# Optimization experiments

Hardware: AMD Instinct MI355X
Metric: run time of the kernel (lower is better)

Reference implementation:

```python
import jax, jax.numpy as jnp
import numpy as np

N, E, G = 50000, 800000, 64          # nodes, edges, graphs
IN, HID, OUT, H = 256, 64, 64, 4     # input dim, per-head hidden, output dim, heads
NEG_SLOPE = 0.2                      # PyG GATConv leaky_relu slope


def _lin(k, fan_in, fan_out):
    return jax.random.normal(k, (fan_in, fan_out), jnp.float32) * (1.0 / np.sqrt(fan_in))


def setup_inputs() -> dict:
    key = jax.random.key(0)
    ks = jax.random.split(key, 16)
    x = jax.random.normal(ks[0], (N, IN), jnp.float32)
    edge_index = jax.random.randint(ks[1], (2, E), 0, N, dtype=jnp.int32)
    batch = jnp.sort(jax.random.randint(ks[2], (N,), 0, G, dtype=jnp.int32))
    # layer 1: IN -> H x HID (concat)
    W1 = _lin(ks[3], IN, H * HID)
    a_src1 = jax.random.normal(ks[4], (H, HID), jnp.float32) * 0.1
    a_dst1 = jax.random.normal(ks[5], (H, HID), jnp.float32) * 0.1
    b1 = jnp.zeros((H * HID,), jnp.float32)
    # layer 2: H*HID -> H x HID (concat)
    W2 = _lin(ks[6], H * HID, H * HID)
    a_src2 = jax.random.normal(ks[7], (H, HID), jnp.float32) * 0.1
    a_dst2 = jax.random.normal(ks[8], (H, HID), jnp.float32) * 0.1
    b2 = jnp.zeros((H * HID,), jnp.float32)
    W3 = _lin(ks[9], H * HID, OUT)
    a_src3 = jax.random.normal(ks[10], (1, OUT), jnp.float32) * 0.1
    a_dst3 = jax.random.normal(ks[11], (1, OUT), jnp.float32) * 0.1
    b3 = jnp.zeros((OUT,), jnp.float32)
    return {"x": x, "edge_index": edge_index, "batch": batch,
            "W1": W1, "a_src1": a_src1, "a_dst1": a_dst1, "b1": b1,
            "W2": W2, "a_src2": a_src2, "a_dst2": a_dst2, "b2": b2,
            "W3": W3, "a_src3": a_src3, "a_dst3": a_dst3, "b3": b3}


def gat_conv(x, src, dst, W, a_src, a_dst, b, heads, out_ch):
    """PyG-style GATConv (eval mode, concat=True semantics; heads=1 == no concat)."""
    n = x.shape[0]
    h = (x @ W).reshape(n, heads, out_ch)                     # [N,H,C]
    alpha_s = jnp.sum(h * a_src, axis=-1)                     # [N,H]
    alpha_d = jnp.sum(h * a_dst, axis=-1)                     # [N,H]
    e = jax.nn.leaky_relu(alpha_s[src] + alpha_d[dst], NEG_SLOPE)  # [E',H]
    # segment softmax over destination nodes (self-loops guarantee nonempty segments)
    m = jax.ops.segment_max(e, dst, num_segments=n)
    e = jnp.exp(e - m[dst])
    denom = jax.ops.segment_sum(e, dst, num_segments=n)
    alpha = e / (denom[dst] + 1e-16)                          # [E',H]
    msg = h[src] * alpha[:, :, None]                          # [E',H,C]
    out = jax.ops.segment_sum(msg, dst, num_segments=n)       # [N,H,C]
    return out.reshape(n, heads * out_ch) + b


def reference(x, edge_index, batch, W1, a_src1, a_dst1, b1, W2, a_src2, a_dst2, b2,
              W3, a_src3, a_dst3, b3):
    n = x.shape[0]
    # GATConv default add_self_loops=True
    loops = jnp.arange(n, dtype=edge_index.dtype)
    src = jnp.concatenate([edge_index[0], loops])
    dst = jnp.concatenate([edge_index[1], loops])

    h = gat_conv(x, src, dst, W1, a_src1, a_dst1, b1, H, HID)
    h = jax.nn.elu(h)  # dropout disabled in eval
    h = gat_conv(h, src, dst, W2, a_src2, a_dst2, b2, H, HID)
    h = jax.nn.elu(h)
    node_embeddings = gat_conv(h, src, dst, W3, a_src3, a_dst3, b3, 1, OUT)

    # global_mean_pool over batch ids
    sums = jax.ops.segment_sum(node_embeddings, batch, num_segments=G)
    counts = jax.ops.segment_sum(jnp.ones((n,), node_embeddings.dtype), batch, num_segments=G)
    graph_embeddings = sums / jnp.maximum(counts, 1.0)[:, None]
    return node_embeddings, graph_embeddings
```

## Files before the change

kernel.cpp:

```cpp
#include <hip/hip_runtime.h>
#include <hip/hip_bf16.h>
#include <hip/hip_fp16.h>

typedef __attribute__((ext_vector_type(8))) _Float16 f16x8;
typedef __attribute__((ext_vector_type(4))) _Float16 f16x4;
typedef __attribute__((ext_vector_type(4))) float f32x4;

static __device__ __forceinline__ void st(float* p, float v)  { *p = v; }
static __device__ __forceinline__ void st(__half* p, float v) { *p = __float2half(v); }

static __device__ __forceinline__ void splitf16(float v, __half& hi, __half& lo) {
    hi = __float2half(v);
    lo = __float2half(v - __half2float(hi));
}

static __device__ __forceinline__ void ldrow4(const __half* p, float* f) {
    const __half2* q = reinterpret_cast<const __half2*>(p);
    float2 a = __half22float2(q[0]), b = __half22float2(q[1]);
    f[0] = a.x; f[1] = a.y; f[2] = b.x; f[3] = b.y;
}
template <int CHUNK>
static __device__ __forceinline__ void ldrow(const __half* p, float* f) {
    if constexpr (CHUNK == 4) ldrow4(p, f); else f[0] = __half2float(*p);
}

__global__ void k_init(int* deg, int N) {
    int i = blockIdx.x * blockDim.x + threadIdx.x;
    if (i < N) deg[i] = 1;
}

__global__ void k_hist(const int* __restrict__ ei, int* deg, int E) {
    int e = blockIdx.x * blockDim.x + threadIdx.x;
    if (e < E) atomicAdd(&deg[ei[E + e]], 1);
}

__global__ void k_scan1(const int* __restrict__ deg, int* __restrict__ offs,
                        int* __restrict__ bsum, int N) {
    __shared__ int sh[256];
    int i = blockIdx.x * 256 + threadIdx.x;
    int v = (i < N) ? deg[i] : 0;
    sh[threadIdx.x] = v;
    __syncthreads();
#pragma unroll
    for (int off = 1; off < 256; off <<= 1) {
        int t = (threadIdx.x >= off) ? sh[threadIdx.x - off] : 0;
        __syncthreads();
        sh[threadIdx.x] += t;
        __syncthreads();
    }
    if (i < N) offs[i] = sh[threadIdx.x] - v;
    if (threadIdx.x == 255) bsum[blockIdx.x] = sh[255];
}

__global__ void k_scan2(int* __restrict__ bsum, int nb) {
    __shared__ int sh[256];
    int v = (threadIdx.x < nb) ? bsum[threadIdx.x] : 0;
    sh[threadIdx.x] = v;
    __syncthreads();
#pragma unroll
    for (int off = 1; off < 256; off <<= 1) {
        int t = (threadIdx.x >= off) ? sh[threadIdx.x - off] : 0;
        __syncthreads();
        sh[threadIdx.x] += t;
        __syncthreads();
    }
    if (threadIdx.x < nb) bsum[threadIdx.x] = sh[threadIdx.x] - v;
    if (threadIdx.x == 255) bsum[nb] = sh[255];
}

__global__ void k_scan3(int* __restrict__ offs, int* __restrict__ cursor,
                        const int* __restrict__ bsum, int N, int nb) {
    int i = blockIdx.x * 256 + threadIdx.x;
    if (i < N) {
        int v = offs[i] + bsum[blockIdx.x];
        offs[i] = v;
        cursor[i] = v;
    }
    if (i == 0) offs[N] = bsum[nb];
}

__global__ void k_scatter(const int* __restrict__ ei, int* cursor, int* csr, int E) {
    int e = blockIdx.x * blockDim.x + threadIdx.x;
    if (e < E) {
        int d = ei[E + e];
        int p = atomicAdd(&cursor[d], 1);
        csr[p] = ei[e];
    }
}

__global__ void k_scatter_loops(int* cursor, int* csr, int N) {
    int i = blockIdx.x * blockDim.x + threadIdx.x;
    if (i < N) { int p = atomicAdd(&cursor[i], 1); csr[p] = i; }
}

__global__ void k_wsplit(const float* __restrict__ W, __half* __restrict__ Wth,
                         __half* __restrict__ Wtl, int K, int M) {
    int idx = blockIdx.x * 256 + threadIdx.x;
    if (idx < K * M) {
        int k = idx / M, n = idx - k * M;
        __half h, l;
        splitf16(W[idx], h, l);
        Wth[(size_t)n * K + k] = h;
        Wtl[(size_t)n * K + k] = l;
    }
}

__global__ void k_xsplit(const float* __restrict__ x, __half* __restrict__ xh,
                         __half* __restrict__ xl, long n4) {
    long i = (long)blockIdx.x * 256 + threadIdx.x;
    if (i < n4) {
        float4 v = *reinterpret_cast<const float4*>(x + i * 4);
        __half h0, h1, h2, h3, l0, l1, l2, l3;
        splitf16(v.x, h0, l0);
        splitf16(v.y, h1, l1);
        splitf16(v.z, h2, l2);
        splitf16(v.w, h3, l3);
        ushort4 hv = { __half_as_ushort(h0), __half_as_ushort(h1),
                       __half_as_ushort(h2), __half_as_ushort(h3) };
        ushort4 lv = { __half_as_ushort(l0), __half_as_ushort(l1),
                       __half_as_ushort(l2), __half_as_ushort(l3) };
        *reinterpret_cast<ushort4*>(xh + i * 4) = hv;
        *reinterpret_cast<ushort4*>(xl + i * 4) = lv;
    }
}

__global__ __launch_bounds__(256) void k_gemm3(const __half* __restrict__ Ah, const __half* __restrict__ Al,
                                               const __half* __restrict__ Wth, const __half* __restrict__ Wtl,
                                               __half* __restrict__ C, int nrows, int K, int M) {
    constexpr int LDA = 40;
    __shared__ __half AH[128 * LDA];
    __shared__ __half AL[128 * LDA];
    __shared__ __half BH[64 * LDA];
    __shared__ __half BL[64 * LDA];

    int tid  = threadIdx.x;
    int lane = tid & 63;
    int wave = tid >> 6;
    int wr = wave & 1, wc = wave >> 1;
    int quad = lane >> 4, r = lane & 15;
    int r0 = blockIdx.x * 128, c0 = blockIdx.y * 64;

    f32x4 acc[4][2];
#pragma unroll
    for (int i = 0; i < 4; ++i)
#pragma unroll
        for (int j = 0; j < 2; ++j) acc[i][j] = (f32x4){0.f, 0.f, 0.f, 0.f};

    for (int kc = 0; kc < K; kc += 32) {
#pragma unroll
        for (int it = 0; it < 2; ++it) {
            int row  = (tid >> 2) + it * 64;
            int kseg = (tid & 3) * 8;
            int gr = r0 + row;
            f16x8 vh = (f16x8)(_Float16)0, vl = (f16x8)(_Float16)0;
            if (gr < nrows) {
                vh = *reinterpret_cast<const f16x8*>(Ah + (size_t)gr * K + kc + kseg);
                vl = *reinterpret_cast<const f16x8*>(Al + (size_t)gr * K + kc + kseg);
            }
            *reinterpret_cast<f16x8*>(&AH[row * LDA + kseg]) = vh;
            *reinterpret_cast<f16x8*>(&AL[row * LDA + kseg]) = vl;
        }
        {
            int n    = tid >> 2;
            int kseg = (tid & 3) * 8;
            *reinterpret_cast<f16x8*>(&BH[n * LDA + kseg]) =
                *reinterpret_cast<const f16x8*>(Wth + (size_t)(c0 + n) * K + kc + kseg);
            *reinterpret_cast<f16x8*>(&BL[n * LDA + kseg]) =
                *reinterpret_cast<const f16x8*>(Wtl + (size_t)(c0 + n) * K + kc + kseg);
        }
        __syncthreads();
        int k0 = quad * 8;
        f16x8 ah[4], al[4], bh[2], bl[2];
#pragma unroll
        for (int tr = 0; tr < 4; ++tr) {
            int row = wr * 64 + tr * 16 + r;
            ah[tr] = *reinterpret_cast<const f16x8*>(&AH[row * LDA + k0]);
            al[tr] = *reinterpret_cast<const f16x8*>(&AL[row * LDA + k0]);
        }
#pragma unroll
        for (int tc = 0; tc < 2; ++tc) {
            int col = wc * 32 + tc * 16 + r;
            bh[tc] = *reinterpret_cast<const f16x8*>(&BH[col * LDA + k0]);
            bl[tc] = *reinterpret_cast<const f16x8*>(&BL[col * LDA + k0]);
        }
#pragma unroll
        for (int tr = 0; tr < 4; ++tr)
#pragma unroll
            for (int tc = 0; tc < 2; ++tc) {
                acc[tr][tc] = __builtin_amdgcn_mfma_f32_16x16x32_f16(ah[tr], bh[tc], acc[tr][tc], 0, 0, 0);
                acc[tr][tc] = __builtin_amdgcn_mfma_f32_16x16x32_f16(ah[tr], bl[tc], acc[tr][tc], 0, 0, 0);
                acc[tr][tc] = __builtin_amdgcn_mfma_f32_16x16x32_f16(al[tr], bh[tc], acc[tr][tc], 0, 0, 0);
            }
        __syncthreads();
    }
#pragma unroll
    for (int tr = 0; tr < 4; ++tr)
#pragma unroll
        for (int tc = 0; tc < 2; ++tc) {
            int col = c0 + wc * 32 + tc * 16 + r;
#pragma unroll
            for (int i = 0; i < 4; ++i) {
                int row = r0 + wr * 64 + tr * 16 + quad * 4 + i;
                if (row < nrows) C[(size_t)row * M + col] = __float2half(acc[tr][tc][i]);
            }
        }
}

__global__ __launch_bounds__(256) void k_gemm2(const __half* __restrict__ A,
                                               const __half* __restrict__ Wth, const __half* __restrict__ Wtl,
                                               __half* __restrict__ C, int nrows, int K, int M) {
    constexpr int LDA = 40;
    __shared__ __half AS[128 * LDA];
    __shared__ __half BH[64 * LDA];
    __shared__ __half BL[64 * LDA];

    int tid  = threadIdx.x;
    int lane = tid & 63;
    int wave = tid >> 6;
    int wr = wave & 1, wc = wave >> 1;
    int quad = lane >> 4, r = lane & 15;
    int r0 = blockIdx.x * 128, c0 = blockIdx.y * 64;

    f32x4 acc[4][2];
#pragma unroll
    for (int i = 0; i < 4; ++i)
#pragma unroll
        for (int j = 0; j < 2; ++j) acc[i][j] = (f32x4){0.f, 0.f, 0.f, 0.f};

    for (int kc = 0; kc < K; kc += 32) {
#pragma unroll
        for (int it = 0; it < 2; ++it) {
            int row  = (tid >> 2) + it * 64;
            int kseg = (tid & 3) * 8;
            int gr = r0 + row;
            f16x8 v = (f16x8)(_Float16)0;
            if (gr < nrows) v = *reinterpret_cast<const f16x8*>(A + (size_t)gr * K + kc + kseg);
            *reinterpret_cast<f16x8*>(&AS[row * LDA + kseg]) = v;
        }
        {
            int n    = tid >> 2;
            int kseg = (tid & 3) * 8;
            *reinterpret_cast<f16x8*>(&BH[n * LDA + kseg]) =
                *reinterpret_cast<const f16x8*>(Wth + (size_t)(c0 + n) * K + kc + kseg);
            *reinterpret_cast<f16x8*>(&BL[n * LDA + kseg]) =
                *reinterpret_cast<const f16x8*>(Wtl + (size_t)(c0 + n) * K + kc + kseg);
        }
        __syncthreads();
        int k0 = quad * 8;
        f16x8 a[4], bh[2], bl[2];
#pragma unroll
        for (int tr = 0; tr < 4; ++tr) {
            int row = wr * 64 + tr * 16 + r;
            a[tr] = *reinterpret_cast<const f16x8*>(&AS[row * LDA + k0]);
        }
#pragma unroll
        for (int tc = 0; tc < 2; ++tc) {
            int col = wc * 32 + tc * 16 + r;
            bh[tc] = *reinterpret_cast<const f16x8*>(&BH[col * LDA + k0]);
            bl[tc] = *reinterpret_cast<const f16x8*>(&BL[col * LDA + k0]);
        }
#pragma unroll
        for (int tr = 0; tr < 4; ++tr)
#pragma unroll
            for (int tc = 0; tc < 2; ++tc) {
                acc[tr][tc] = __builtin_amdgcn_mfma_f32_16x16x32_f16(a[tr], bh[tc], acc[tr][tc], 0, 0, 0);
                acc[tr][tc] = __builtin_amdgcn_mfma_f32_16x16x32_f16(a[tr], bl[tc], acc[tr][tc], 0, 0, 0);
            }
        __syncthreads();
    }
#pragma unroll
    for (int tr = 0; tr < 4; ++tr)
#pragma unroll
        for (int tc = 0; tc < 2; ++tc) {
            int col = c0 + wc * 32 + tc * 16 + r;
#pragma unroll
            for (int i = 0; i < 4; ++i) {
                int row = r0 + wr * 64 + tr * 16 + quad * 4 + i;
                if (row < nrows) C[(size_t)row * M + col] = __float2half(acc[tr][tc][i]);
            }
        }
}

template <int CHUNK>
__global__ void k_alpha(const __half* __restrict__ feat, const float* __restrict__ a_src,
                        const float* __restrict__ a_dst, float* __restrict__ als,
                        float* __restrict__ ald, int N) {
    constexpr int M = 64 * CHUNK;
    constexpr int H = M / 64;
    constexpr int WIDTH = 64 / H;
    int lane = threadIdx.x & 63;
    int node = blockIdx.x * 4 + (threadIdx.x >> 6);
    if (node >= N) return;
    float f[CHUNK];
    ldrow<CHUNK>(feat + (size_t)node * M + lane * CHUNK, f);
    float ps = 0.f, pd = 0.f;
#pragma unroll
    for (int j = 0; j < CHUNK; ++j) {
        int col = lane * CHUNK + j;
        ps += f[j] * a_src[col];
        pd += f[j] * a_dst[col];
    }
#pragma unroll
    for (int off = 1; off < WIDTH; off <<= 1) {
        ps += __shfl_xor(ps, off, 64);
        pd += __shfl_xor(pd, off, 64);
    }
    if ((lane & (WIDTH - 1)) == 0) {
        int head = lane / WIDTH;
        als[(size_t)node * H + head] = ps;
        ald[(size_t)node * H + head] = pd;
    }
}

template <int CHUNK, bool ELU, typename OT>
__global__ void k_agg(const __half* __restrict__ feat, const int* __restrict__ offs,
                      const int* __restrict__ csr, const float* __restrict__ als,
                      const float* __restrict__ ald, const float* __restrict__ bias,
                      OT* __restrict__ out, int N) {
    constexpr int M  = 64 * CHUNK;
    constexpr int H  = (CHUNK == 4) ? 4 : 1;
    constexpr int EC = 16;
    constexpr int SH = (CHUNK == 4) ? 9 : 7;

    __shared__ float    shw[4][2][64];
    __shared__ unsigned sho[4][2][EC];

    int tid  = threadIdx.x;
    int lane = tid & 63;
    int wid  = tid >> 6;
    int node = blockIdx.x * 4 + wid;
    if (node >= N) return;

    int ia = lane & 15;
    int ha = (H == 4) ? (lane >> 4) : 0;
    int ho = lane >> 4;

    float adv = ald[(size_t)node * H + ha];

    int beg = offs[node], end = offs[node + 1];
    int d   = end - beg;
    int nc  = (d + EC - 1) >> 4;

    const char* fbase = reinterpret_cast<const char*>(feat) + lane * (CHUNK * 2);

    float acc[CHUNK] = {};
    float den = 0.f;

    int sv = csr[beg + min(ia, min(EC, d) - 1)];
    float xv = als[(size_t)sv * H + ha];
    int sv_n = sv;
    if (nc > 1) {
        int cn = min(EC, d - EC);
        sv_n = csr[beg + EC + min(ia, cn - 1)];
    }

    for (int c = 0; c < nc; ++c) {
        int cnt = min(EC, d - c * EC);

        float e = xv + adv;
        e = (e > 0.f) ? e : 0.2f * e;
        float w = (ia < cnt) ? __expf(e) : 0.f;
        den += w;
        int b = c & 1;
        shw[wid][b][lane] = w;
        if (lane < EC) sho[wid][b][lane] = (unsigned)sv << SH;

        xv = als[(size_t)sv_n * H + ha];
        sv = sv_n;
        if (c + 2 < nc) {
            int cn = min(EC, d - (c + 2) * EC);
            sv_n = csr[beg + (c + 2) * EC + min(ia, cn - 1)];
        }

        const float* wp = &shw[wid][b][ho * EC];
        float4 w0 = *reinterpret_cast<const float4*>(wp);
        float4 w1 = *reinterpret_cast<const float4*>(wp + 4);
        float4 w2 = *reinterpret_cast<const float4*>(wp + 8);
        float4 w3 = *reinterpret_cast<const float4*>(wp + 12);
        const unsigned* op = &sho[wid][b][0];
        uint4 o0 = *reinterpret_cast<const uint4*>(op);
        uint4 o1 = *reinterpret_cast<const uint4*>(op + 4);
        uint4 o2 = *reinterpret_cast<const uint4*>(op + 8);
        uint4 o3 = *reinterpret_cast<const uint4*>(op + 12);
        float    ww[EC] = {w0.x, w0.y, w0.z, w0.w, w1.x, w1.y, w1.z, w1.w,
                           w2.x, w2.y, w2.z, w2.w, w3.x, w3.y, w3.z, w3.w};
        unsigned oo[EC] = {o0.x, o0.y, o0.z, o0.w, o1.x, o1.y, o1.z, o1.w,
                           o2.x, o2.y, o2.z, o2.w, o3.x, o3.y, o3.z, o3.w};
        if constexpr (CHUNK == 4) {
            f16x4 v[EC];
#pragma unroll
            for (int t = 0; t < EC; ++t)
                v[t] = *reinterpret_cast<const f16x4*>(fbase + oo[t]);
#pragma unroll
            for (int t = 0; t < EC; ++t)
#pragma unroll
                for (int j = 0; j < 4; ++j)
                    acc[j] = fmaf((float)v[t][j], ww[t], acc[j]);
        } else {
            __half v[EC];
#pragma unroll
            for (int t = 0; t < EC; ++t)
                v[t] = *reinterpret_cast<const __half*>(fbase + oo[t]);
#pragma unroll
            for (int t = 0; t < EC; ++t)
                acc[0] = fmaf(__half2float(v[t]), ww[t], acc[0]);
        }
    }

#pragma unroll
    for (int off = 1; off < EC; off <<= 1) den += __shfl_xor(den, off, 64);
    float inv = 1.f / (den + 1e-16f);

#pragma unroll
    for (int j = 0; j < CHUNK; ++j) {
        int col = lane * CHUNK + j;
        float v = acc[j] * inv + bias[col];
        if (ELU) v = (v > 0.f) ? v : (__expf(v) - 1.f);
        st(&out[(size_t)node * M + col], v);
    }
}

static __device__ __forceinline__ int lowerb(const int* __restrict__ a, int n, int v) {
    int lo = 0, hi = n;
    while (lo < hi) { int mid = (lo + hi) >> 1; if (a[mid] < v) lo = mid + 1; else hi = mid; }
    return lo;
}

__global__ void k_pool2(const float* __restrict__ ne, const int* __restrict__ batch,
                        float* __restrict__ gout, int N) {
    int g = blockIdx.x;
    int lo = lowerb(batch, N, g);
    int hi = lowerb(batch, N, g + 1);
    int lane = threadIdx.x & 63, row = threadIdx.x >> 6;
    float s = 0.f;
    for (int i = lo + row; i < hi; i += 4) s += ne[(size_t)i * 64 + lane];
    __shared__ float red[4][64];
    red[row][lane] = s;
    __syncthreads();
    if (row == 0) {
        float v = red[0][lane] + red[1][lane] + red[2][lane] + red[3][lane];
        gout[(size_t)g * 64 + lane] = v / fmaxf((float)(hi - lo), 1.f);
    }
}

extern "C" void kernel_launch(void* const* d_in, const int* in_sizes, int n_in,
                              void* d_out, int out_size, void* d_ws, size_t ws_size,
                              hipStream_t stream) {
    const float* x   = (const float*)d_in[0];
    const int* ei    = (const int*)d_in[1];
    const int* batch = (const int*)d_in[2];
    const float* W1  = (const float*)d_in[3];
    const float* as1 = (const float*)d_in[4];
    const float* ad1 = (const float*)d_in[5];
    const float* b1  = (const float*)d_in[6];
    const float* W2  = (const float*)d_in[7];
    const float* as2 = (const float*)d_in[8];
    const float* ad2 = (const float*)d_in[9];
    const float* b2  = (const float*)d_in[10];
    const float* W3  = (const float*)d_in[11];
    const float* as3 = (const float*)d_in[12];
    const float* ad3 = (const float*)d_in[13];
    const float* b3  = (const float*)d_in[14];

    const int N = in_sizes[2];
    const int E = in_sizes[1] / 2;
    const int G = 64;
    float* out = (float*)d_out;

    char* w = (char*)d_ws;
    auto carve = [&](size_t bytes) { char* p = w; w += (bytes + 255) & ~(size_t)255; return p; };
    __half* feat = (__half*)carve((size_t)N * 256 * 2);
    __half* xh   = (__half*)carve((size_t)N * 256 * 2);
    __half* xl   = (__half*)carve((size_t)N * 256 * 2);
    __half* act  = xh;
    float* als   = (float*)carve((size_t)N * 4 * 4);
    float* ald   = (float*)carve((size_t)N * 4 * 4);
    int* deg     = (int*)carve((size_t)N * 4);
    int* offs    = (int*)carve((size_t)(N + 1) * 4);
    int* cursor  = (int*)carve((size_t)N * 4);
    int* csr     = (int*)carve((size_t)(E + N) * 4);
    int nb       = (N + 255) / 256;
    int* bsum    = (int*)carve((size_t)(nb + 1) * 4);
    __half* w1h  = (__half*)carve((size_t)256 * 256 * 2);
    __half* w1l  = (__half*)carve((size_t)256 * 256 * 2);
    __half* w2h  = (__half*)carve((size_t)256 * 256 * 2);
    __half* w2l  = (__half*)carve((size_t)256 * 256 * 2);
    __half* w3h  = (__half*)carve((size_t)256 * 64 * 2);
    __half* w3l  = (__half*)carve((size_t)256 * 64 * 2);

    k_init<<<(N + 255) / 256, 256, 0, stream>>>(deg, N);
    k_hist<<<(E + 255) / 256, 256, 0, stream>>>(ei, deg, E);
    k_scan1<<<nb, 256, 0, stream>>>(deg, offs, bsum, N);
    k_scan2<<<1, 256, 0, stream>>>(bsum, nb);
    k_scan3<<<nb, 256, 0, stream>>>(offs, cursor, bsum, N, nb);
    k_scatter<<<(E + 255) / 256, 256, 0, stream>>>(ei, cursor, csr, E);
    k_scatter_loops<<<(N + 255) / 256, 256, 0, stream>>>(cursor, csr, N);

    k_wsplit<<<(256 * 256 + 255) / 256, 256, 0, stream>>>(W1, w1h, w1l, 256, 256);
    k_wsplit<<<(256 * 256 + 255) / 256, 256, 0, stream>>>(W2, w2h, w2l, 256, 256);
    k_wsplit<<<(256 * 64 + 255) / 256, 256, 0, stream>>>(W3, w3h, w3l, 256, 64);
    long n4 = (long)N * 64;
    k_xsplit<<<(int)((n4 + 255) / 256), 256, 0, stream>>>(x, xh, xl, n4);

    dim3 gemmBig((N + 127) / 128, 4);
    dim3 gemmSmall((N + 127) / 128, 1);
    int nodeBlocks = (N + 3) / 4;

    k_gemm3<<<gemmBig, 256, 0, stream>>>(xh, xl, w1h, w1l, feat, N, 256, 256);
    k_alpha<4><<<nodeBlocks, 256, 0, stream>>>(feat, as1, ad1, als, ald, N);
    k_agg<4, true, __half><<<nodeBlocks, 256, 0, stream>>>(feat, offs, csr, als, ald, b1, act, N);
    k_gemm2<<<gemmBig, 256, 0, stream>>>(act, w2h, w2l, feat, N, 256, 256);
    k_alpha<4><<<nodeBlocks, 256, 0, stream>>>(feat, as2, ad2, als, ald, N);
    k_agg<4, true, __half><<<nodeBlocks, 256, 0, stream>>>(feat, offs, csr, als, ald, b2, act, N);
    k_gemm2<<<gemmSmall, 256, 0, stream>>>(act, w3h, w3l, feat, N, 256, 64);
    k_alpha<1><<<nodeBlocks, 256, 0, stream>>>(feat, as3, ad3, als, ald, N);
    k_agg<1, false, float><<<nodeBlocks, 256, 0, stream>>>(feat, offs, csr, als, ald, b3, out, N);

    k_pool2<<<G, 256, 0, stream>>>(out, batch, out + (size_t)N * 64, N);
}
```

Measured before the change: 558.3 us.

## Fuse attention-logit computation into GEMM epilogue and merge setup kernels

Each GEMM block now computes the per-node source and destination attention dot products in its epilogue. It reduces them across lanes with shuffles and across waves through LDS reused from the A tile, then writes them to als and ald. This removes the three separate k_alpha kernels, which re-read the whole feature matrix. The setup path is also consolidated: the self-loop increment moves into the scan, the loop scatter is merged into the edge scatter, and the three weight-split launches become one. This cuts launch count at the cost of a little extra epilogue work and one extra block-wide barrier.

```diff
diff --git a/kernel.cpp b/kernel.cpp
--- a/kernel.cpp
+++ b/kernel.cpp
@@ -12,21 +12,6 @@
 static __device__ __forceinline__ void splitf16(float v, __half& hi, __half& lo) {
     hi = __float2half(v);
     lo = __float2half(v - __half2float(hi));
-}
-
-static __device__ __forceinline__ void ldrow4(const __half* p, float* f) {
-    const __half2* q = reinterpret_cast<const __half2*>(p);
-    float2 a = __half22float2(q[0]), b = __half22float2(q[1]);
-    f[0] = a.x; f[1] = a.y; f[2] = b.x; f[3] = b.y;
-}
-template <int CHUNK>
-static __device__ __forceinline__ void ldrow(const __half* p, float* f) {
-    if constexpr (CHUNK == 4) ldrow4(p, f); else f[0] = __half2float(*p);
-}
-
-__global__ void k_init(int* deg, int N) {
-    int i = blockIdx.x * blockDim.x + threadIdx.x;
-    if (i < N) deg[i] = 1;
 }
 
 __global__ void k_hist(const int* __restrict__ ei, int* deg, int E) {
@@ -38,7 +23,7 @@
                         int* __restrict__ bsum, int N) {
     __shared__ int sh[256];
     int i = blockIdx.x * 256 + threadIdx.x;
-    int v = (i < N) ? deg[i] : 0;
+    int v = (i < N) ? (deg[i] + 1) : 0;
     sh[threadIdx.x] = v;
     __syncthreads();
 #pragma unroll
@@ -79,30 +64,37 @@
     if (i == 0) offs[N] = bsum[nb];
 }
 
-__global__ void k_scatter(const int* __restrict__ ei, int* cursor, int* csr, int E) {
+__global__ void k_scatter_all(const int* __restrict__ ei, int* cursor, int* csr,
+                              int E, int N) {
     int e = blockIdx.x * blockDim.x + threadIdx.x;
     if (e < E) {
         int d = ei[E + e];
         int p = atomicAdd(&cursor[d], 1);
         csr[p] = ei[e];
-    }
-}
-
-__global__ void k_scatter_loops(int* cursor, int* csr, int N) {
-    int i = blockIdx.x * blockDim.x + threadIdx.x;
-    if (i < N) { int p = atomicAdd(&cursor[i], 1); csr[p] = i; }
-}
-
-__global__ void k_wsplit(const float* __restrict__ W, __half* __restrict__ Wth,
-                         __half* __restrict__ Wtl, int K, int M) {
+    } else if (e < E + N) {
+        int i = e - E;
+        int p = atomicAdd(&cursor[i], 1);
+        csr[p] = i;
+    }
+}
+
+__global__ void k_wsplit_all(const float* __restrict__ W1, const float* __restrict__ W2,
+                             const float* __restrict__ W3,
+                             __half* __restrict__ w1h, __half* __restrict__ w1l,
+                             __half* __restrict__ w2h, __half* __restrict__ w2l,
+                             __half* __restrict__ w3h, __half* __restrict__ w3l) {
     int idx = blockIdx.x * 256 + threadIdx.x;
-    if (idx < K * M) {
-        int k = idx / M, n = idx - k * M;
-        __half h, l;
-        splitf16(W[idx], h, l);
-        Wth[(size_t)n * K + k] = h;
-        Wtl[(size_t)n * K + k] = l;
-    }
+    const float* W; __half *Wh, *Wl; int M, base;
+    constexpr int K = 256;
+    if (idx < 65536)       { W = W1; Wh = w1h; Wl = w1l; M = 256; base = idx; }
+    else if (idx < 131072) { W = W2; Wh = w2h; Wl = w2l; M = 256; base = idx - 65536; }
+    else if (idx < 147456) { W = W3; Wh = w3h; Wl = w3l; M = 64;  base = idx - 131072; }
+    else return;
+    int k = base / M, n = base - k * M;
+    __half h, l;
+    splitf16(W[base], h, l);
+    Wh[(size_t)n * K + k] = h;
+    Wl[(size_t)n * K + k] = l;
 }
 
 __global__ void k_xsplit(const float* __restrict__ x, __half* __restrict__ xh,
@@ -124,9 +116,68 @@
     }
 }
 
+template <typename ACC>
+static __device__ __forceinline__ void alpha_epilogue(
+        const ACC& acc, float* ldsf, const float* __restrict__ a_src,
+        const float* __restrict__ a_dst, float* __restrict__ als,
+        float* __restrict__ ald, __half* __restrict__ C,
+        int nrows, int M, int H, int r0, int c0,
+        int wr, int wc, int quad, int r, int tid) {
+    float ps[4][4], pd[4][4];
+#pragma unroll
+    for (int tr = 0; tr < 4; ++tr)
+#pragma unroll
+        for (int i = 0; i < 4; ++i) { ps[tr][i] = 0.f; pd[tr][i] = 0.f; }
+
+#pragma unroll
+    for (int tr = 0; tr < 4; ++tr)
+#pragma unroll
+        for (int tc = 0; tc < 2; ++tc) {
+            int col = c0 + wc * 32 + tc * 16 + r;
+            float av_s = a_src[col], av_d = a_dst[col];
+#pragma unroll
+            for (int i = 0; i < 4; ++i) {
+                int row = r0 + wr * 64 + tr * 16 + quad * 4 + i;
+                __half hv = __float2half(acc[tr][tc][i]);
+                float vr = __half2float(hv);
+                if (row < nrows) C[(size_t)row * M + col] = hv;
+                ps[tr][i] = fmaf(vr, av_s, ps[tr][i]);
+                pd[tr][i] = fmaf(vr, av_d, pd[tr][i]);
+            }
+        }
+#pragma unroll
+    for (int tr = 0; tr < 4; ++tr)
+#pragma unroll
+        for (int i = 0; i < 4; ++i) {
+            float s = ps[tr][i], d2 = pd[tr][i];
+#pragma unroll
+            for (int off = 1; off < 16; off <<= 1) {
+                s  += __shfl_xor(s,  off, 64);
+                d2 += __shfl_xor(d2, off, 64);
+            }
+            if (r == 0) {
+                int lrow = wr * 64 + tr * 16 + quad * 4 + i;
+                ldsf[(0 * 2 + wc) * 128 + lrow] = s;
+                ldsf[(2 + wc) * 128 + lrow]     = d2;
+            }
+        }
+    __syncthreads();
+    int lrow = tid >> 1, which = tid & 1;
+    if (lrow < 128) {
+        float v = ldsf[(which * 2 + 0) * 128 + lrow] + ldsf[(which * 2 + 1) * 128 + lrow];
+        int grow = r0 + lrow;
+        if (grow < nrows) {
+            float* dst = which ? ald : als;
+            dst[(size_t)grow * H + (c0 >> 6)] = v;
+        }
+    }
+}
+
 __global__ __launch_bounds__(256) void k_gemm3(const __half* __restrict__ Ah, const __half* __restrict__ Al,
                                                const __half* __restrict__ Wth, const __half* __restrict__ Wtl,
-                                               __half* __restrict__ C, int nrows, int K, int M) {
+                                               __half* __restrict__ C, int nrows, int K, int M,
+                                               const float* __restrict__ a_src, const float* __restrict__ a_dst,
+                                               float* __restrict__ als, float* __restrict__ ald, int H) {
     constexpr int LDA = 40;
     __shared__ __half AH[128 * LDA];
     __shared__ __half AL[128 * LDA];
@@ -193,22 +244,15 @@
             }
         __syncthreads();
     }
-#pragma unroll
-    for (int tr = 0; tr < 4; ++tr)
-#pragma unroll
-        for (int tc = 0; tc < 2; ++tc) {
-            int col = c0 + wc * 32 + tc * 16 + r;
-#pragma unroll
-            for (int i = 0; i < 4; ++i) {
-                int row = r0 + wr * 64 + tr * 16 + quad * 4 + i;
-                if (row < nrows) C[(size_t)row * M + col] = __float2half(acc[tr][tc][i]);
-            }
-        }
+    alpha_epilogue(acc, reinterpret_cast<float*>(AH), a_src, a_dst, als, ald, C,
+                   nrows, M, H, r0, c0, wr, wc, quad, r, tid);
 }
 
 __global__ __launch_bounds__(256) void k_gemm2(const __half* __restrict__ A,
                                                const __half* __restrict__ Wth, const __half* __restrict__ Wtl,
-                                               __half* __restrict__ C, int nrows, int K, int M) {
+                                               __half* __restrict__ C, int nrows, int K, int M,
+                                               const float* __restrict__ a_src, const float* __restrict__ a_dst,
+                                               float* __restrict__ als, float* __restrict__ ald, int H) {
     constexpr int LDA = 40;
     __shared__ __half AS[128 * LDA];
     __shared__ __half BH[64 * LDA];
@@ -268,48 +312,8 @@
             }
         __syncthreads();
     }
-#pragma unroll
-    for (int tr = 0; tr < 4; ++tr)
-#pragma unroll
-        for (int tc = 0; tc < 2; ++tc) {
-            int col = c0 + wc * 32 + tc * 16 + r;
-#pragma unroll
-            for (int i = 0; i < 4; ++i) {
-                int row = r0 + wr * 64 + tr * 16 + quad * 4 + i;
-                if (row < nrows) C[(size_t)row * M + col] = __float2half(acc[tr][tc][i]);
-            }
-        }
-}
-
-template <int CHUNK>
-__global__ void k_alpha(const __half* __restrict__ feat, const float* __restrict__ a_src,
-                        const float* __restrict__ a_dst, float* __restrict__ als,
-                        float* __restrict__ ald, int N) {
-    constexpr int M = 64 * CHUNK;
-    constexpr int H = M / 64;
-    constexpr int WIDTH = 64 / H;
-    int lane = threadIdx.x & 63;
-    int node = blockIdx.x * 4 + (threadIdx.x >> 6);
-    if (node >= N) return;
-    float f[CHUNK];
-    ldrow<CHUNK>(feat + (size_t)node * M + lane * CHUNK, f);
-    float ps = 0.f, pd = 0.f;
-#pragma unroll
-    for (int j = 0; j < CHUNK; ++j) {
-        int col = lane * CHUNK + j;
-        ps += f[j] * a_src[col];
-        pd += f[j] * a_dst[col];
-    }
-#pragma unroll
-    for (int off = 1; off < WIDTH; off <<= 1) {
-        ps += __shfl_xor(ps, off, 64);
-        pd += __shfl_xor(pd, off, 64);
-    }
-    if ((lane & (WIDTH - 1)) == 0) {
-        int head = lane / WIDTH;
-        als[(size_t)node * H + head] = ps;
-        ald[(size_t)node * H + head] = pd;
-    }
+    alpha_epilogue(acc, reinterpret_cast<float*>(AS), a_src, a_dst, als, ald, C,
+                   nrows, M, H, r0, c0, wr, wc, quad, r, tid);
 }
 
 template <int CHUNK, bool ELU, typename OT>
@@ -488,17 +492,14 @@
     __half* w3h  = (__half*)carve((size_t)256 * 64 * 2);
     __half* w3l  = (__half*)carve((size_t)256 * 64 * 2);
 
-    k_init<<<(N + 255) / 256, 256, 0, stream>>>(deg, N);
+    hipMemsetAsync(deg, 0, (size_t)N * 4, stream);
     k_hist<<<(E + 255) / 256, 256, 0, stream>>>(ei, deg, E);
     k_scan1<<<nb, 256, 0, stream>>>(deg, offs, bsum, N);
     k_scan2<<<1, 256, 0, stream>>>(bsum, nb);
     k_scan3<<<nb, 256, 0, stream>>>(offs, cursor, bsum, N, nb);
-    k_scatter<<<(E + 255) / 256, 256, 0, stream>>>(ei, cursor, csr, E);
-    k_scatter_loops<<<(N + 255) / 256, 256, 0, stream>>>(cursor, csr, N);
-
-    k_wsplit<<<(256 * 256 + 255) / 256, 256, 0, stream>>>(W1, w1h, w1l, 256, 256);
-    k_wsplit<<<(256 * 256 + 255) / 256, 256, 0, stream>>>(W2, w2h, w2l, 256, 256);
-    k_wsplit<<<(256 * 64 + 255) / 256, 256, 0, stream>>>(W3, w3h, w3l, 256, 64);
+    k_scatter_all<<<(E + N + 255) / 256, 256, 0, stream>>>(ei, cursor, csr, E, N);
+
+    k_wsplit_all<<<(147456 + 255) / 256, 256, 0, stream>>>(W1, W2, W3, w1h, w1l, w2h, w2l, w3h, w3l);
     long n4 = (long)N * 64;
     k_xsplit<<<(int)((n4 + 255) / 256), 256, 0, stream>>>(x, xh, xl, n4);
 
@@ -506,14 +507,14 @@
     dim3 gemmSmall((N + 127) / 128, 1);
     int nodeBlocks = (N + 3) / 4;
 
-    k_gemm3<<<gemmBig, 256, 0, stream>>>(xh, xl, w1h, w1l, feat, N, 256, 256);
-    k_alpha<4><<<nodeBlocks, 256, 0, stream>>>(feat, as1, ad1, als, ald, N);
+    k_gemm3<<<gemmBig, 256, 0, stream>>>(xh, xl, w1h, w1l, feat, N, 256, 256,
+                                         as1, ad1, als, ald, 4);
     k_agg<4, true, __half><<<nodeBlocks, 256, 0, stream>>>(feat, offs, csr, als, ald, b1, act, N);
-    k_gemm2<<<gemmBig, 256, 0, stream>>>(act, w2h, w2l, feat, N, 256, 256);
-    k_alpha<4><<<nodeBlocks, 256, 0, stream>>>(feat, as2, ad2, als, ald, N);
+    k_gemm2<<<gemmBig, 256, 0, stream>>>(act, w2h, w2l, feat, N, 256, 256,
+                                         as2, ad2, als, ald, 4);
     k_agg<4, true, __half><<<nodeBlocks, 256, 0, stream>>>(feat, offs, csr, als, ald, b2, act, N);
-    k_gemm2<<<gemmSmall, 256, 0, stream>>>(act, w3h, w3l, feat, N, 256, 64);
-    k_alpha<1><<<nodeBlocks, 256, 0, stream>>>(feat, as3, ad3, als, ald, N);
+    k_gemm2<<<gemmSmall, 256, 0, stream>>>(act, w3h, w3l, feat, N, 256, 64,
+                                           as3, ad3, als, ald, 1);
     k_agg<1, false, float><<<nodeBlocks, 256, 0, stream>>>(feat, offs, csr, als, ald, b3, out, N);
 
     k_pool2<<<G, 256, 0, stream>>>(out, batch, out + (size_t)N * 64, N);
```

Result: faster. 541.0 us (-3.1%).
